# Kernel tuning notes

Measured on AMD Instinct MI355X. Metric: run time of the kernel, lower is better.

## Reference

```python
import jax, jax.numpy as jnp
import numpy as np

NC, NU, K, C, P, O = 20, 16, 128, 2048, 5, 256

def setup_inputs() -> dict:
    key = jax.random.key(0)
    ks = jax.random.split(key, 6)
    s = 0.02  # keep activations well-scaled
    return {
        "topk_feats": jax.random.normal(ks[0], (NC, NU, K, C), jnp.float32),
        "prototypes": jax.random.normal(ks[1], (NC, P, C), jnp.float32),
        "w_inner1": jax.random.normal(ks[2], (O, C), jnp.float32) * s,
        "w_inner_trans": jax.random.normal(ks[3], (C, C), jnp.float32) * s,
        "w_inter1": jax.random.normal(ks[4], (O, C), jnp.float32) * s,
        "w_inter2": jax.random.normal(ks[5], (O, C), jnp.float32) * s,
    }

def reference(topk_feats, prototypes, w_inner1, w_inner_trans, w_inter1, w_inter2):
    scale = 1.0 / jnp.sqrt(jnp.asarray(O, topk_feats.dtype))
    # --- inner (per-group) self-attention, vmapped over (class, unlabel) ---
    # fe: [nc, nu, k, o]
    fe = jnp.einsum("nukc,oc->nuko", topk_feats, w_inner1)
    att = jax.nn.softmax(jnp.einsum("nuko,nulo->nukl", fe, fe) * scale, axis=-1)
    agg = jnp.einsum("nukl,nulc->nukc", att, topk_feats)  # atte @ feat
    feats = topk_feats + jax.nn.relu(jnp.einsum("nukc,dc->nukd", agg, w_inner_trans))
    # --- inter (prototype -> all feats) cross-attention per class ---
    fa = feats.reshape(NC, NU * K, C)  # cat over unlabel dim
    fae = jnp.einsum("nmc,oc->nmo", fa, w_inter1)
    pe = jnp.einsum("npc,oc->npo", prototypes, w_inter2)
    att2 = jax.nn.softmax(jnp.einsum("npo,nmo->npm", pe, fae) * scale, axis=-1)
    un_protos = jnp.einsum("npm,nmc->npc", att2, fa)  # [nc, p, c]
    return un_protos
```

## Files before the change

### kernel.cpp

```cpp
#include <hip/hip_runtime.h>

typedef __attribute__((ext_vector_type(4))) float f32x4;
typedef __attribute__((ext_vector_type(8))) short short8;

#define DEVI static __device__ __forceinline__

DEVI unsigned short f2bf(float f) {
  unsigned int u = __float_as_uint(f);
  u += 0x7FFFu + ((u >> 16) & 1u);
  return (unsigned short)(u >> 16);
}
DEVI float bf2f(unsigned short s) { return __uint_as_float(((unsigned int)s) << 16); }
DEVI unsigned int pack2(float lo, float hi) {
  return ((unsigned int)f2bf(hi) << 16) | (unsigned int)f2bf(lo);
}

#define GL2LDS(gp, lp)                                                        \
  __builtin_amdgcn_global_load_lds(                                           \
      (const __attribute__((address_space(1))) void*)(const void*)(gp),       \
      (__attribute__((address_space(3))) void*)(void*)(lp), 16, 0, 0)

__global__ __launch_bounds__(256) void k_cvt_bf16(const float* __restrict__ src,
                                                  unsigned short* __restrict__ dst, int n4) {
  int i = blockIdx.x * 256 + threadIdx.x;
  if (i < n4) {
    float4 v = ((const float4*)src)[i];
    uint2 o; o.x = pack2(v.x, v.y); o.y = pack2(v.z, v.w);
    ((uint2*)dst)[i] = o;
  }
}

template <bool RES>
__global__ __launch_bounds__(256) void k_gemm_bt(const unsigned short* __restrict__ A,
                                                 const unsigned short* __restrict__ B,
                                                 unsigned short* __restrict__ C,
                                                 const float* __restrict__ resid, int N) {
  constexpr int K = 2048;
  __shared__ unsigned short lA[128 * 64];
  __shared__ unsigned short lB[128 * 64];
  const int tid = threadIdx.x;
  const int lane = tid & 63;
  const int wave = tid >> 6;
  const int wr = wave >> 1, wc = wave & 1;
  const long mBase = (long)blockIdx.y * 128;
  const long nBase = (long)blockIdx.x * 128;

  f32x4 acc[4][4] = {};

  for (int k0 = 0; k0 < K; k0 += 64) {
    __syncthreads();
#pragma unroll
    for (int it = 0; it < 4; it++) {
      int idx = it * 256 + wave * 64 + lane;
      int row = idx >> 3;
      int kc = idx & 7;
      int skc = kc ^ (row & 7);
      const unsigned short* ga = A + (mBase + row) * (long)K + k0 + skc * 8;
      const unsigned short* gb = B + (nBase + row) * (long)K + k0 + skc * 8;
      int lbase = (it * 256 + wave * 64) * 8;
      GL2LDS(ga, &lA[lbase]);
      GL2LDS(gb, &lB[lbase]);
    }
    __syncthreads();
#pragma unroll
    for (int kb = 0; kb < 2; kb++) {
      short8 af[4], bfr[4];
#pragma unroll
      for (int mt = 0; mt < 4; mt++) {
        int row = wr * 64 + mt * 16 + (lane & 15);
        int slot = (kb * 4 + (lane >> 4)) ^ (row & 7);
        af[mt] = *(const short8*)&lA[row * 64 + slot * 8];
      }
#pragma unroll
      for (int nt = 0; nt < 4; nt++) {
        int row = wc * 64 + nt * 16 + (lane & 15);
        int slot = (kb * 4 + (lane >> 4)) ^ (row & 7);
        bfr[nt] = *(const short8*)&lB[row * 64 + slot * 8];
      }
#pragma unroll
      for (int mt = 0; mt < 4; mt++)
#pragma unroll
        for (int nt = 0; nt < 4; nt++)
          acc[mt][nt] = __builtin_amdgcn_mfma_f32_16x16x32_bf16(af[mt], bfr[nt], acc[mt][nt], 0, 0, 0);
    }
  }
#pragma unroll
  for (int mt = 0; mt < 4; mt++) {
#pragma unroll
    for (int nt = 0; nt < 4; nt++) {
#pragma unroll
      for (int j = 0; j < 4; j++) {
        long row = mBase + wr * 64 + mt * 16 + (lane >> 4) * 4 + j;
        long col = nBase + wc * 64 + nt * 16 + (lane & 15);
        float v = acc[mt][nt][j];
        if constexpr (RES) v = resid[row * (long)N + col] + fmaxf(v, 0.0f);
        C[row * (long)N + col] = f2bf(v);
      }
    }
  }
}

__global__ __launch_bounds__(256) void k_attn_inner(const unsigned short* __restrict__ fe,
                                                    const unsigned short* __restrict__ topkb,
                                                    unsigned short* __restrict__ agg) {
  __shared__ unsigned short attb[128 * 136];
  __shared__ unsigned short featT[64 * 128];
  __shared__ float redmax[2 * 128];
  __shared__ float redsum[2 * 128];
  const int tid = threadIdx.x;
  const int lane = tid & 63;
  const int wave = tid >> 6;
  const int wr = wave >> 1, wc = wave & 1;
  const int g = blockIdx.x;
  const unsigned short* feG = fe + (long)g * 128 * 256;

  f32x4 s[4][4] = {};
#pragma unroll
  for (int kb = 0; kb < 8; kb++) {
    short8 af[4], bfr[4];
#pragma unroll
    for (int mt = 0; mt < 4; mt++) {
      int row = wr * 64 + mt * 16 + (lane & 15);
      af[mt] = *(const short8*)(feG + row * 256 + kb * 32 + (lane >> 4) * 8);
    }
#pragma unroll
    for (int nt = 0; nt < 4; nt++) {
      int row = wc * 64 + nt * 16 + (lane & 15);
      bfr[nt] = *(const short8*)(feG + row * 256 + kb * 32 + (lane >> 4) * 8);
    }
#pragma unroll
    for (int mt = 0; mt < 4; mt++)
#pragma unroll
      for (int nt = 0; nt < 4; nt++)
        s[mt][nt] = __builtin_amdgcn_mfma_f32_16x16x32_bf16(af[mt], bfr[nt], s[mt][nt], 0, 0, 0);
  }

  const float cexp = 0.0625f * 1.44269504088896f;
#pragma unroll
  for (int mt = 0; mt < 4; mt++) {
#pragma unroll
    for (int j = 0; j < 4; j++) {
      float m = fmaxf(fmaxf(s[mt][0][j], s[mt][1][j]), fmaxf(s[mt][2][j], s[mt][3][j]));
#pragma unroll
      for (int d = 1; d < 16; d <<= 1) m = fmaxf(m, __shfl_xor(m, d, 64));
      int r = wr * 64 + mt * 16 + (lane >> 4) * 4 + j;
      if ((lane & 15) == 0) redmax[wc * 128 + r] = m;
    }
  }
  __syncthreads();
#pragma unroll
  for (int mt = 0; mt < 4; mt++) {
#pragma unroll
    for (int j = 0; j < 4; j++) {
      int r = wr * 64 + mt * 16 + (lane >> 4) * 4 + j;
      float M = fmaxf(redmax[r], redmax[128 + r]);
      float sm = 0.f;
#pragma unroll
      for (int nt = 0; nt < 4; nt++) {
        float p = exp2f((s[mt][nt][j] - M) * cexp);
        s[mt][nt][j] = p;
        sm += p;
      }
#pragma unroll
      for (int d = 1; d < 16; d <<= 1) sm += __shfl_xor(sm, d, 64);
      if ((lane & 15) == 0) redsum[wc * 128 + r] = sm;
    }
  }
  __syncthreads();
#pragma unroll
  for (int mt = 0; mt < 4; mt++) {
#pragma unroll
    for (int j = 0; j < 4; j++) {
      int r = wr * 64 + mt * 16 + (lane >> 4) * 4 + j;
      float inv = 1.0f / (redsum[r] + redsum[128 + r]);
#pragma unroll
      for (int nt = 0; nt < 4; nt++) {
        int c = wc * 64 + nt * 16 + (lane & 15);
        attb[r * 136 + c] = f2bf(s[mt][nt][j] * inv);
      }
    }
  }

  for (int ch = 0; ch < 32; ch++) {
    __syncthreads();
#pragma unroll
    for (int i = 0; i < 4; i++) {
      int seg = i * 256 + tid;
      int l = seg >> 3, kc = seg & 7;
      const unsigned short* gp = topkb + ((long)g * 128 + l) * 2048 + ch * 64 + kc * 8;
      uint4 w = *(const uint4*)gp;
      unsigned short v[8];
      v[0] = (unsigned short)(w.x & 0xffff); v[1] = (unsigned short)(w.x >> 16);
      v[2] = (unsigned short)(w.y & 0xffff); v[3] = (unsigned short)(w.y >> 16);
      v[4] = (unsigned short)(w.z & 0xffff); v[5] = (unsigned short)(w.z >> 16);
      v[6] = (unsigned short)(w.w & 0xffff); v[7] = (unsigned short)(w.w >> 16);
      int lx = l ^ (kc << 3);
#pragma unroll
      for (int j = 0; j < 8; j++) featT[(kc * 8 + j) * 128 + lx] = v[j];
    }
    __syncthreads();
    f32x4 c[2][4] = {};
#pragma unroll
    for (int kb = 0; kb < 4; kb++) {
      short8 af2[2], bf2v[4];
#pragma unroll
      for (int mt = 0; mt < 2; mt++) {
        int r = wave * 32 + mt * 16 + (lane & 15);
        af2[mt] = *(const short8*)&attb[r * 136 + kb * 32 + (lane >> 4) * 8];
      }
#pragma unroll
      for (int nt = 0; nt < 4; nt++) {
        int cc = nt * 16 + (lane & 15);
        int l0 = (kb * 32 + (lane >> 4) * 8) ^ (((cc >> 3) & 7) << 3);
        bf2v[nt] = *(const short8*)&featT[cc * 128 + l0];
      }
#pragma unroll
      for (int mt = 0; mt < 2; mt++)
#pragma unroll
        for (int nt = 0; nt < 4; nt++)
          c[mt][nt] = __builtin_amdgcn_mfma_f32_16x16x32_bf16(af2[mt], bf2v[nt], c[mt][nt], 0, 0, 0);
    }
#pragma unroll
    for (int mt = 0; mt < 2; mt++)
#pragma unroll
      for (int nt = 0; nt < 4; nt++)
#pragma unroll
        for (int j = 0; j < 4; j++) {
          long row = (long)g * 128 + wave * 32 + mt * 16 + (lane >> 4) * 4 + j;
          int col = ch * 64 + nt * 16 + (lane & 15);
          agg[row * 2048 + col] = f2bf(c[mt][nt][j]);
        }
  }
}

__global__ __launch_bounds__(256) void k_pe(const float* __restrict__ protos,
                                            const float* __restrict__ wi2,
                                            float* __restrict__ pe) {
  int n = blockIdx.x, oc = blockIdx.y, tid = threadIdx.x;
  if (tid < 160) {
    int p = tid >> 5, o = oc * 32 + (tid & 31);
    const float* pr = protos + ((long)n * 5 + p) * 2048;
    const float* wr = wi2 + (long)o * 2048;
    float acc = 0.f;
    for (int cidx = 0; cidx < 2048; cidx += 4) {
      float4 a = *(const float4*)(pr + cidx);
      float4 b = *(const float4*)(wr + cidx);
      acc += a.x * b.x + a.y * b.y + a.z * b.z + a.w * b.w;
    }
    pe[((long)n * 5 + p) * 256 + o] = acc;
  }
}

__global__ __launch_bounds__(256) void k_logits(const float* __restrict__ pe,
                                                const unsigned short* __restrict__ fae,
                                                float* __restrict__ lg) {
  __shared__ float pel[5 * 256];
  int n = blockIdx.x, mc = blockIdx.y, tid = threadIdx.x;
  for (int i = tid; i < 1280; i += 256) pel[i] = pe[(long)n * 1280 + i];
  __syncthreads();
  int m = mc * 256 + tid;
  const unsigned short* fr = fae + ((long)n * 2048 + m) * 256;
  float a[5] = {0.f, 0.f, 0.f, 0.f, 0.f};
  for (int o = 0; o < 256; o += 8) {
    uint4 w = *(const uint4*)(fr + o);
    float f[8];
    f[0] = bf2f((unsigned short)(w.x & 0xffff)); f[1] = bf2f((unsigned short)(w.x >> 16));
    f[2] = bf2f((unsigned short)(w.y & 0xffff)); f[3] = bf2f((unsigned short)(w.y >> 16));
    f[4] = bf2f((unsigned short)(w.z & 0xffff)); f[5] = bf2f((unsigned short)(w.z >> 16));
    f[6] = bf2f((unsigned short)(w.w & 0xffff)); f[7] = bf2f((unsigned short)(w.w >> 16));
#pragma unroll
    for (int j = 0; j < 8; j++) {
      float fv = f[j];
#pragma unroll
      for (int p = 0; p < 5; p++) a[p] += fv * pel[p * 256 + o + j];
    }
  }
#pragma unroll
  for (int p = 0; p < 5; p++) lg[((long)n * 5 + p) * 2048 + m] = a[p] * 0.0625f;
}

__global__ __launch_bounds__(256) void k_sm(const float* __restrict__ lg,
                                            float* __restrict__ att2) {
  __shared__ float red[4], red2[4];
  int b = blockIdx.x, tid = threadIdx.x;
  const float* src = lg + (long)b * 2048;
  float v[8];
  float mx = -1e30f;
#pragma unroll
  for (int i = 0; i < 8; i++) { v[i] = src[i * 256 + tid]; mx = fmaxf(mx, v[i]); }
#pragma unroll
  for (int d = 1; d < 64; d <<= 1) mx = fmaxf(mx, __shfl_xor(mx, d, 64));
  if ((tid & 63) == 0) red[tid >> 6] = mx;
  __syncthreads();
  mx = fmaxf(fmaxf(red[0], red[1]), fmaxf(red[2], red[3]));
  float sm = 0.f;
#pragma unroll
  for (int i = 0; i < 8; i++) { v[i] = exp2f((v[i] - mx) * 1.44269504088896f); sm += v[i]; }
#pragma unroll
  for (int d = 1; d < 64; d <<= 1) sm += __shfl_xor(sm, d, 64);
  if ((tid & 63) == 0) red2[tid >> 6] = sm;
  __syncthreads();
  float inv = 1.0f / (red2[0] + red2[1] + red2[2] + red2[3]);
  float* dst = att2 + (long)b * 2048;
#pragma unroll
  for (int i = 0; i < 8; i++) dst[i * 256 + tid] = v[i] * inv;
}

__global__ __launch_bounds__(256) void k_out_part(const float* __restrict__ att2,
                                                  const unsigned short* __restrict__ feats,
                                                  float* __restrict__ partial) {
  __shared__ float a2[5 * 512];
  int n = blockIdx.x, cb = blockIdx.y, ms = blockIdx.z;
  int tid = threadIdx.x;
  const float* src = att2 + (long)n * 5 * 2048 + ms * 512;
  for (int i = tid; i < 640; i += 256) {
    int p = i >> 7, q = i & 127;
    ((float4*)a2)[i] = *(const float4*)(src + p * 2048 + q * 4);
  }
  __syncthreads();
  int c0 = cb * 1024 + tid * 4;
  const unsigned short* fp = feats + ((long)n * 2048 + ms * 512) * 2048 + c0;
  float acc[5][4] = {};
  for (int m = 0; m < 512; m++) {
    uint2 w = *(const uint2*)(fp + (long)m * 2048);
    float f0 = bf2f((unsigned short)(w.x & 0xffff));
    float f1 = bf2f((unsigned short)(w.x >> 16));
    float f2 = bf2f((unsigned short)(w.y & 0xffff));
    float f3 = bf2f((unsigned short)(w.y >> 16));
#pragma unroll
    for (int p = 0; p < 5; p++) {
      float a = a2[p * 512 + m];
      acc[p][0] += a * f0; acc[p][1] += a * f1; acc[p][2] += a * f2; acc[p][3] += a * f3;
    }
  }
  float* pp = partial + ((long)ms * 100 + (long)n * 5) * 2048;
#pragma unroll
  for (int p = 0; p < 5; p++) {
    float4 o; o.x = acc[p][0]; o.y = acc[p][1]; o.z = acc[p][2]; o.w = acc[p][3];
    *(float4*)(pp + p * 2048 + c0) = o;
  }
}

__global__ __launch_bounds__(256) void k_out_red(const float* __restrict__ partial,
                                                 float* __restrict__ outp) {
  int i = blockIdx.x * 256 + threadIdx.x;
  const f32x4* P = (const f32x4*)partial;
  f32x4 s = P[i] + P[51200 + i] + P[2 * 51200 + i] + P[3 * 51200 + i];
  ((f32x4*)outp)[i] = s;
}

extern "C" void kernel_launch(void* const* d_in, const int* in_sizes, int n_in,
                              void* d_out, int out_size, void* d_ws, size_t ws_size,
                              hipStream_t stream) {
  const float* topk = (const float*)d_in[0];
  const float* protos = (const float*)d_in[1];
  const float* w1 = (const float*)d_in[2];
  const float* wt = (const float*)d_in[3];
  const float* wi1 = (const float*)d_in[4];
  const float* wi2 = (const float*)d_in[5];
  float* outp = (float*)d_out;

  char* ws = (char*)d_ws;
  size_t off = 0;
  auto alloc = [&](size_t bytes) -> void* {
    void* p = ws + off;
    off += (bytes + 255) & ~(size_t)255;
    return p;
  };
  unsigned short* w1b = (unsigned short*)alloc((size_t)256 * 2048 * 2);
  unsigned short* wtb = (unsigned short*)alloc((size_t)2048 * 2048 * 2);
  unsigned short* wi1b = (unsigned short*)alloc((size_t)256 * 2048 * 2);
  unsigned short* topkb = (unsigned short*)alloc((size_t)40960 * 2048 * 2);
  unsigned short* fe = (unsigned short*)alloc((size_t)40960 * 256 * 2);
  unsigned short* agg = (unsigned short*)alloc((size_t)40960 * 2048 * 2);
  float* pe = (float*)alloc((size_t)20 * 5 * 256 * 4);
  float* lg = (float*)alloc((size_t)20 * 5 * 2048 * 4);
  float* att2 = (float*)alloc((size_t)20 * 5 * 2048 * 4);
  float* partial = (float*)alloc((size_t)4 * 20 * 5 * 2048 * 4);
  unsigned short* feats = topkb;
  unsigned short* fae = fe;

  k_cvt_bf16<<<512, 256, 0, stream>>>(w1, w1b, 131072);
  k_cvt_bf16<<<4096, 256, 0, stream>>>(wt, wtb, 1048576);
  k_cvt_bf16<<<512, 256, 0, stream>>>(wi1, wi1b, 131072);
  k_cvt_bf16<<<81920, 256, 0, stream>>>(topk, topkb, 20971520);

  k_gemm_bt<false><<<dim3(2, 320), 256, 0, stream>>>(topkb, w1b, fe, nullptr, 256);
  k_attn_inner<<<320, 256, 0, stream>>>(fe, topkb, agg);
  k_gemm_bt<true><<<dim3(16, 320), 256, 0, stream>>>(agg, wtb, feats, topk, 2048);
  k_gemm_bt<false><<<dim3(2, 320), 256, 0, stream>>>(feats, wi1b, fae, nullptr, 256);
  k_pe<<<dim3(20, 8), 256, 0, stream>>>(protos, wi2, pe);
  k_logits<<<dim3(20, 8), 256, 0, stream>>>(pe, fae, lg);
  k_sm<<<100, 256, 0, stream>>>(lg, att2);
  k_out_part<<<dim3(20, 2, 4), 256, 0, stream>>>(att2, feats, partial);
  k_out_red<<<200, 256, 0, stream>>>(partial, outp);
}
```

Measured before the change: 1.032 ms.

## Fold inter projection into prototype query and use 256x256 tile GEMM

Replaces the fae GEMM (feats times w_inter1) with an algebraic reordering: project the prototype embeddings back through w_inter1 to get q, then compute logits directly as feats dot q. This removes a 40960x256x2048 GEMM and the wi1 bf16 conversion, at the cost of k_lg reading full 2048-wide feats rows with scalar FMAs. It also adds a new 512-thread GEMM kernel with 256x256 tiles, double-buffered direct-to-LDS loads and swizzled LDS, replacing the old tile GEMM for the large residual transform. Precision changes slightly because q is kept in fp32 instead of going through a bf16 fae.

```diff
diff --git a/kernel.cpp b/kernel.cpp
--- a/kernel.cpp
+++ b/kernel.cpp
@@ -100,6 +100,88 @@
   }
 }
 
+template <bool RES>
+__global__ __launch_bounds__(512, 2) void k_gemm256(const unsigned short* __restrict__ A,
+                                                    const unsigned short* __restrict__ B,
+                                                    unsigned short* __restrict__ C,
+                                                    const float* __restrict__ resid, int N) {
+  constexpr int K = 2048;
+  __shared__ unsigned short lA[2][256 * 64];
+  __shared__ unsigned short lB[2][256 * 64];
+  const int tid = threadIdx.x;
+  const int lane = tid & 63;
+  const int wave = tid >> 6;
+  const int wr = wave >> 2, wc = wave & 3;
+  const long mBase = (long)blockIdx.y * 256;
+  const long nBase = (long)blockIdx.x * 256;
+
+  f32x4 acc[8][4] = {};
+
+  auto stage = [&](int buf, int k0) {
+#pragma unroll
+    for (int it = 0; it < 4; it++) {
+      int idx = it * 512 + tid;
+      int row = idx >> 3, kc = idx & 7;
+      int skc = kc ^ (row & 7);
+      int lbase = (it * 512 + (tid & ~63)) * 8;
+      GL2LDS(A + (mBase + row) * (long)K + k0 + skc * 8, &lA[buf][lbase]);
+      GL2LDS(B + (nBase + row) * (long)K + k0 + skc * 8, &lB[buf][lbase]);
+    }
+  };
+
+  stage(0, 0);
+  for (int t = 0; t < 32; t++) {
+    const int cur = t & 1;
+    if (t < 31) {
+      stage(cur ^ 1, (t + 1) * 64);
+      asm volatile("s_waitcnt vmcnt(8)" ::: "memory");
+    } else {
+      asm volatile("s_waitcnt vmcnt(0)" ::: "memory");
+    }
+    __builtin_amdgcn_s_barrier();
+    __builtin_amdgcn_sched_barrier(0);
+    const unsigned short* bA = &lA[cur][0];
+    const unsigned short* bB = &lB[cur][0];
+#pragma unroll
+    for (int kb = 0; kb < 2; kb++) {
+      short8 af[8], bfr[4];
+#pragma unroll
+      for (int mt = 0; mt < 8; mt++) {
+        int row = wr * 128 + mt * 16 + (lane & 15);
+        int slot = (kb * 4 + (lane >> 4)) ^ (row & 7);
+        af[mt] = *(const short8*)&bA[row * 64 + slot * 8];
+      }
+#pragma unroll
+      for (int nt = 0; nt < 4; nt++) {
+        int row = wc * 64 + nt * 16 + (lane & 15);
+        int slot = (kb * 4 + (lane >> 4)) ^ (row & 7);
+        bfr[nt] = *(const short8*)&bB[row * 64 + slot * 8];
+      }
+#pragma unroll
+      for (int mt = 0; mt < 8; mt++)
+#pragma unroll
+        for (int nt = 0; nt < 4; nt++)
+          acc[mt][nt] = __builtin_amdgcn_mfma_f32_16x16x32_bf16(af[mt], bfr[nt], acc[mt][nt], 0, 0, 0);
+    }
+    __builtin_amdgcn_sched_barrier(0);
+    __builtin_amdgcn_s_barrier();
+  }
+#pragma unroll
+  for (int mt = 0; mt < 8; mt++) {
+#pragma unroll
+    for (int nt = 0; nt < 4; nt++) {
+#pragma unroll
+      for (int j = 0; j < 4; j++) {
+        long row = mBase + wr * 128 + mt * 16 + (lane >> 4) * 4 + j;
+        long col = nBase + wc * 64 + nt * 16 + (lane & 15);
+        float v = acc[mt][nt][j];
+        if constexpr (RES) v = resid[row * (long)N + col] + fmaxf(v, 0.0f);
+        C[row * (long)N + col] = f2bf(v);
+      }
+    }
+  }
+}
+
 __global__ __launch_bounds__(256) void k_attn_inner(const unsigned short* __restrict__ fe,
                                                     const unsigned short* __restrict__ topkb,
                                                     unsigned short* __restrict__ agg) {
@@ -251,18 +333,37 @@
   }
 }
 
-__global__ __launch_bounds__(256) void k_logits(const float* __restrict__ pe,
-                                                const unsigned short* __restrict__ fae,
-                                                float* __restrict__ lg) {
-  __shared__ float pel[5 * 256];
+__global__ __launch_bounds__(256) void k_q(const float* __restrict__ pe,
+                                           const float* __restrict__ wi1,
+                                           float* __restrict__ q) {
+  __shared__ float pel[1280];
+  int n = blockIdx.x, cb = blockIdx.y, tid = threadIdx.x;
+  for (int i = tid; i < 1280; i += 256) pel[i] = pe[(long)n * 1280 + i];
+  __syncthreads();
+  int c = cb * 256 + tid;
+  float a[5] = {0.f, 0.f, 0.f, 0.f, 0.f};
+  for (int o = 0; o < 256; o++) {
+    float w = wi1[(long)o * 2048 + c];
+#pragma unroll
+    for (int p = 0; p < 5; p++) a[p] += pel[p * 256 + o] * w;
+  }
+#pragma unroll
+  for (int p = 0; p < 5; p++) q[((long)n * 5 + p) * 2048 + c] = a[p];
+}
+
+__global__ __launch_bounds__(256) void k_lg(const float* __restrict__ q,
+                                            const unsigned short* __restrict__ feats,
+                                            float* __restrict__ lg) {
+  __shared__ float ql[5 * 2048];
   int n = blockIdx.x, mc = blockIdx.y, tid = threadIdx.x;
-  for (int i = tid; i < 1280; i += 256) pel[i] = pe[(long)n * 1280 + i];
+  const float* qs = q + (long)n * 5 * 2048;
+  for (int i = tid; i < 2560; i += 256) ((float4*)ql)[i] = ((const float4*)qs)[i];
   __syncthreads();
   int m = mc * 256 + tid;
-  const unsigned short* fr = fae + ((long)n * 2048 + m) * 256;
+  const unsigned short* fr = feats + ((long)n * 2048 + m) * 2048;
   float a[5] = {0.f, 0.f, 0.f, 0.f, 0.f};
-  for (int o = 0; o < 256; o += 8) {
-    uint4 w = *(const uint4*)(fr + o);
+  for (int c = 0; c < 2048; c += 8) {
+    uint4 w = *(const uint4*)(fr + c);
     float f[8];
     f[0] = bf2f((unsigned short)(w.x & 0xffff)); f[1] = bf2f((unsigned short)(w.x >> 16));
     f[2] = bf2f((unsigned short)(w.y & 0xffff)); f[3] = bf2f((unsigned short)(w.y >> 16));
@@ -272,7 +373,7 @@
     for (int j = 0; j < 8; j++) {
       float fv = f[j];
 #pragma unroll
-      for (int p = 0; p < 5; p++) a[p] += fv * pel[p * 256 + o + j];
+      for (int p = 0; p < 5; p++) a[p] += fv * ql[p * 2048 + c + j];
     }
   }
 #pragma unroll
@@ -314,8 +415,8 @@
   int tid = threadIdx.x;
   const float* src = att2 + (long)n * 5 * 2048 + ms * 512;
   for (int i = tid; i < 640; i += 256) {
-    int p = i >> 7, q = i & 127;
-    ((float4*)a2)[i] = *(const float4*)(src + p * 2048 + q * 4);
+    int p = i >> 7, qq = i & 127;
+    ((float4*)a2)[i] = *(const float4*)(src + p * 2048 + qq * 4);
   }
   __syncthreads();
   int c0 = cb * 1024 + tid * 4;
@@ -369,28 +470,26 @@
   };
   unsigned short* w1b = (unsigned short*)alloc((size_t)256 * 2048 * 2);
   unsigned short* wtb = (unsigned short*)alloc((size_t)2048 * 2048 * 2);
-  unsigned short* wi1b = (unsigned short*)alloc((size_t)256 * 2048 * 2);
   unsigned short* topkb = (unsigned short*)alloc((size_t)40960 * 2048 * 2);
   unsigned short* fe = (unsigned short*)alloc((size_t)40960 * 256 * 2);
   unsigned short* agg = (unsigned short*)alloc((size_t)40960 * 2048 * 2);
   float* pe = (float*)alloc((size_t)20 * 5 * 256 * 4);
+  float* q = (float*)alloc((size_t)20 * 5 * 2048 * 4);
   float* lg = (float*)alloc((size_t)20 * 5 * 2048 * 4);
   float* att2 = (float*)alloc((size_t)20 * 5 * 2048 * 4);
   float* partial = (float*)alloc((size_t)4 * 20 * 5 * 2048 * 4);
   unsigned short* feats = topkb;
-  unsigned short* fae = fe;
 
   k_cvt_bf16<<<512, 256, 0, stream>>>(w1, w1b, 131072);
   k_cvt_bf16<<<4096, 256, 0, stream>>>(wt, wtb, 1048576);
-  k_cvt_bf16<<<512, 256, 0, stream>>>(wi1, wi1b, 131072);
   k_cvt_bf16<<<81920, 256, 0, stream>>>(topk, topkb, 20971520);
 
   k_gemm_bt<false><<<dim3(2, 320), 256, 0, stream>>>(topkb, w1b, fe, nullptr, 256);
   k_attn_inner<<<320, 256, 0, stream>>>(fe, topkb, agg);
-  k_gemm_bt<true><<<dim3(16, 320), 256, 0, stream>>>(agg, wtb, feats, topk, 2048);
-  k_gemm_bt<false><<<dim3(2, 320), 256, 0, stream>>>(feats, wi1b, fae, nullptr, 256);
+  k_gemm256<true><<<dim3(8, 160), 512, 0, stream>>>(agg, wtb, feats, topk, 2048);
   k_pe<<<dim3(20, 8), 256, 0, stream>>>(protos, wi2, pe);
-  k_logits<<<dim3(20, 8), 256, 0, stream>>>(pe, fae, lg);
+  k_q<<<dim3(20, 8), 256, 0, stream>>>(pe, wi1, q);
+  k_lg<<<dim3(20, 8), 256, 0, stream>>>(q, feats, lg);
   k_sm<<<100, 256, 0, stream>>>(lg, att2);
   k_out_part<<<dim3(20, 2, 4), 256, 0, stream>>>(att2, feats, partial);
   k_out_red<<<200, 256, 0, stream>>>(partial, outp);
```

Result: no change. 1.041 ms (+0.9%).
